# Optimization experiments

Hardware: AMD Instinct MI355X
Metric: run time of the kernel (lower is better)

Reference implementation:

```python
import jax, jax.numpy as jnp
import numpy as np

B, N, ENC = 64, 49, 1024
DEC, EMB, V = 512, 512, 10000
NT = 4            # num templates -> policy head dim = 1 + NT = 5
MS, MW = 8, 20    # max_sentences, max_words


def setup_inputs() -> dict:
    key = jax.random.key(0)
    ks = jax.random.split(key, 26)
    p = lambda k, shp: jax.random.normal(k, shp, dtype=jnp.float32) * 0.05
    return {
        'spatial_features': jax.random.normal(ks[0], (B, N, ENC), dtype=jnp.float32),
        'target_words': jax.random.randint(ks[1], (B, MS, MW), 0, V, dtype=jnp.int32),
        'emb_W': p(ks[2], (V, EMB)),
        's_W_ih': p(ks[3], (3 * DEC, ENC)),
        's_W_hh': p(ks[4], (3 * DEC, DEC)),
        's_b_ih': p(ks[5], (3 * DEC,)),
        's_b_hh': p(ks[6], (3 * DEC,)),
        'policy_W': p(ks[7], (1 + NT, DEC)),
        'policy_b': p(ks[8], (1 + NT,)),
        'stop_W': p(ks[9], (1, DEC)),
        'stop_b': p(ks[10], (1,)),
        'att_enc_W': p(ks[11], (EMB, ENC)),
        'att_enc_b': p(ks[12], (EMB,)),
        'att_dec_W': p(ks[13], (EMB, DEC)),
        'att_dec_b': p(ks[14], (EMB,)),
        'att_full_W': p(ks[15], (1, EMB)),
        'att_full_b': p(ks[16], (1,)),
        'w_W_ih': p(ks[17], (3 * DEC, EMB + ENC)),
        'w_W_hh': p(ks[18], (3 * DEC, DEC)),
        'w_b_ih': p(ks[19], (3 * DEC,)),
        'w_b_hh': p(ks[20], (3 * DEC,)),
        'fc_W': p(ks[21], (V, DEC)),
        'fc_b': p(ks[22], (V,)),
        'init_W': p(ks[23], (DEC, ENC)),
        'init_b': p(ks[24], (DEC,)),
    }


def _gru_cell(x, h, W_ih, W_hh, b_ih, b_hh):
    # torch.nn.GRUCell semantics
    gi = x @ W_ih.T + b_ih          # [B, 3D]
    gh = h @ W_hh.T + b_hh          # [B, 3D]
    i_r, i_z, i_n = jnp.split(gi, 3, axis=1)
    h_r, h_z, h_n = jnp.split(gh, 3, axis=1)
    r = jax.nn.sigmoid(i_r + h_r)
    z = jax.nn.sigmoid(i_z + h_z)
    n = jnp.tanh(i_n + r * h_n)
    return (1.0 - z) * n + z * h


def reference(spatial_features, target_words, emb_W,
              s_W_ih, s_W_hh, s_b_ih, s_b_hh,
              policy_W, policy_b, stop_W, stop_b,
              att_enc_W, att_enc_b, att_dec_W, att_dec_b, att_full_W, att_full_b,
              w_W_ih, w_W_hh, w_b_ih, w_b_hh,
              fc_W, fc_b, init_W, init_b):
    b = spatial_features.shape[0]
    global_features = spatial_features.mean(axis=1)                 # [B, ENC]
    h_s = jnp.tanh(global_features @ init_W.T + init_b)             # [B, DEC]
    # encoder attention projection is constant across all steps
    att1 = spatial_features @ att_enc_W.T + att_enc_b               # [B, N, EMB]

    def word_step(h_w, emb_t):
        att2 = h_w @ att_dec_W.T + att_dec_b                        # [B, EMB]
        e = jax.nn.relu(att1 + att2[:, None, :]) @ att_full_W[0] + att_full_b[0]  # [B, N]
        alpha = jax.nn.softmax(e, axis=1)
        ctx = jnp.einsum('bn,bnc->bc', alpha, spatial_features)     # [B, ENC]
        x = jnp.concatenate([emb_t, ctx], axis=1)                   # [B, EMB+ENC]
        h_new = _gru_cell(x, h_w, w_W_ih, w_W_hh, w_b_ih, w_b_hh)
        logits = h_new @ fc_W.T + fc_b                              # [B, V]
        return h_new, logits

    bos = jnp.full((b, 1), 1, dtype=target_words.dtype)
    policy_l, stop_l, word_l = [], [], []
    for i in range(MS):
        h_s = _gru_cell(global_features, h_s, s_W_ih, s_W_hh, s_b_ih, s_b_hh)
        policy_l.append(h_s @ policy_W.T + policy_b)
        stop_l.append(h_s @ stop_W.T + stop_b)
        # teacher forcing: input word at t is target[t-1], t=0 uses BOS(=1)
        prev = jnp.concatenate([bos, target_words[:, i, :-1]], axis=1)   # [B, MW]
        embs = jnp.swapaxes(emb_W[prev], 0, 1)                           # [MW, B, EMB]
        _, sent_logits = jax.lax.scan(word_step, h_s, embs)              # [MW, B, V]
        word_l.append(jnp.swapaxes(sent_logits, 0, 1))                   # [B, MW, V]

    return (jnp.stack(policy_l, axis=1),   # [B, MS, 1+NT]
            jnp.stack(stop_l, axis=1),     # [B, MS, 1]
            jnp.stack(word_l, axis=1))     # [B, MS, MW, V]
```

## Files before the change

### kernel.cpp

```cpp
#include <hip/hip_runtime.h>
#include <cmath>

constexpr int B = 64, N_SP = 49, ENC = 1024, DEC = 512, EMB = 512, V = 10000;
constexpr int MS = 8, MW = 20;
constexpr int BW = B * MS;
constexpr int XDIM = EMB + ENC;

__global__ void mean_kernel(const float* __restrict__ sp, float* __restrict__ g) {
    int b = blockIdx.x;
    for (int c = threadIdx.x; c < ENC; c += blockDim.x) {
        float s = 0.f;
        for (int n = 0; n < N_SP; ++n) s += sp[(size_t)(b * N_SP + n) * ENC + c];
        g[b * ENC + c] = s * (1.0f / 49.0f);
    }
}

template <int BM, int BN, int BK, int TM, int TN, int ACT, int SCATTER>
__launch_bounds__(256)
__global__ void gemm_tn(const float* __restrict__ A, int lda,
                        const float* __restrict__ W, int ldw,
                        const float* __restrict__ bias,
                        float* __restrict__ C, int ldc,
                        int M, int N, int K) {
    __shared__ float As[BK][BM + 4];
    __shared__ float Ws[BK][BN + 4];
    const int tid = threadIdx.x;
    const int tx = tid % (BN / TN);
    const int ty = tid / (BN / TN);
    const int m0 = blockIdx.y * BM, n0 = blockIdx.x * BN;

    float acc[TM][TN];
#pragma unroll
    for (int i = 0; i < TM; ++i)
#pragma unroll
        for (int j = 0; j < TN; ++j) acc[i][j] = 0.f;

    constexpr int Q = BK / 4;
    const int arow = tid / Q, akq = (tid % Q) * 4;
    const int wrow = tid / Q, wkq = (tid % Q) * 4;

    for (int k0 = 0; k0 < K; k0 += BK) {
        float4 av = make_float4(0.f, 0.f, 0.f, 0.f);
        float4 wv = make_float4(0.f, 0.f, 0.f, 0.f);
        int gr = m0 + arow;
        if (gr < M) av = *reinterpret_cast<const float4*>(&A[(size_t)gr * lda + k0 + akq]);
        int gn = n0 + wrow;
        if (gn < N) wv = *reinterpret_cast<const float4*>(&W[(size_t)gn * ldw + k0 + wkq]);
        __syncthreads();
        As[akq + 0][arow] = av.x; As[akq + 1][arow] = av.y;
        As[akq + 2][arow] = av.z; As[akq + 3][arow] = av.w;
        Ws[wkq + 0][wrow] = wv.x; Ws[wkq + 1][wrow] = wv.y;
        Ws[wkq + 2][wrow] = wv.z; Ws[wkq + 3][wrow] = wv.w;
        __syncthreads();
#pragma unroll
        for (int kk = 0; kk < BK; ++kk) {
            float a[TM], w[TN];
#pragma unroll
            for (int i = 0; i < TM; ++i) a[i] = As[kk][ty * TM + i];
#pragma unroll
            for (int j = 0; j < TN; ++j) w[j] = Ws[kk][tx * TN + j];
#pragma unroll
            for (int i = 0; i < TM; ++i)
#pragma unroll
                for (int j = 0; j < TN; ++j) acc[i][j] += a[i] * w[j];
        }
        __syncthreads();
    }

#pragma unroll
    for (int i = 0; i < TM; ++i) {
        int r = m0 + ty * TM + i;
        if (r >= M) continue;
#pragma unroll
        for (int j = 0; j < TN; ++j) {
            int n = n0 + tx * TN + j;
            if (n >= N) continue;
            float v = acc[i][j] + bias[n];
            if (ACT == 1) v = tanhf(v);
            size_t off;
            if (SCATTER) {
                int bb = r & 63, tt = (r >> 6) % MW, ss = r / (64 * MW);
                off = (size_t)((bb * MS + ss) * MW + tt) * ldc + n;
            } else {
                off = (size_t)r * ldc + n;
            }
            C[off] = v;
        }
    }
}

__global__ void gru_combine(const float* __restrict__ gi, const float* __restrict__ gh,
                            const float* __restrict__ hprev, float* __restrict__ hout,
                            float* __restrict__ hout2, int M, int t, int word_mode) {
    int idx = blockIdx.x * blockDim.x + threadIdx.x;
    if (idx >= M * DEC) return;
    int r = idx / DEC, c = idx % DEC;
    size_t g0 = (size_t)r * 3 * DEC + c;
    float ir = gi[g0], iz = gi[g0 + DEC], in_ = gi[g0 + 2 * DEC];
    float hr = gh[g0], hz = gh[g0 + DEC], hn = gh[g0 + 2 * DEC];
    float rr = 1.f / (1.f + expf(-(ir + hr)));
    float zz = 1.f / (1.f + expf(-(iz + hz)));
    float nn = tanhf(in_ + rr * hn);
    float h = (1.f - zz) * nn + zz * hprev[(size_t)r * DEC + c];
    hout[(size_t)r * DEC + c] = h;
    if (hout2) {
        int r2 = word_mode ? (((r >> 6) * MW + t) << 6) + (r & 63) : r;
        hout2[(size_t)r2 * DEC + c] = h;
    }
}

__launch_bounds__(256)
__global__ void attn_kernel(const float* __restrict__ sp, const float* __restrict__ att1,
                            const float* __restrict__ att2, const float* __restrict__ wfull,
                            const float* __restrict__ bfull, const float* __restrict__ embW,
                            const int* __restrict__ tw, float* __restrict__ x, int t) {
    int r = blockIdx.x;
    int s = r >> 6, b = r & 63;
    __shared__ float a2[EMB];
    __shared__ float wf[EMB];
    __shared__ float alpha[64];
    int tid = threadIdx.x;
    for (int c = tid; c < EMB; c += 256) {
        a2[c] = att2[(size_t)r * EMB + c];
        wf[c] = wfull[c];
    }
    __syncthreads();
    int wave = tid >> 6, lane = tid & 63;
    for (int n = wave; n < N_SP; n += 4) {
        float acc = 0.f;
        const float* a1p = &att1[(size_t)(b * N_SP + n) * EMB];
        for (int c0 = 0; c0 < EMB; c0 += 64) {
            float v = a1p[c0 + lane] + a2[c0 + lane];
            v = fmaxf(v, 0.f);
            acc += v * wf[c0 + lane];
        }
        for (int m = 32; m; m >>= 1) acc += __shfl_xor(acc, m, 64);
        if (lane == 0) alpha[n] = acc + bfull[0];
    }
    __syncthreads();
    if (tid < 64) {
        float e = (tid < N_SP) ? alpha[tid] : -1e30f;
        float mx = e;
        for (int m = 32; m; m >>= 1) mx = fmaxf(mx, __shfl_xor(mx, m, 64));
        float p = (tid < N_SP) ? expf(e - mx) : 0.f;
        float sum = p;
        for (int m = 32; m; m >>= 1) sum += __shfl_xor(sum, m, 64);
        if (tid < N_SP) alpha[tid] = p / sum;
    }
    __syncthreads();
    for (int c = tid; c < ENC; c += 256) {
        float acc = 0.f;
        const float* spb = &sp[(size_t)b * N_SP * ENC + c];
#pragma unroll 7
        for (int n = 0; n < N_SP; ++n) acc += alpha[n] * spb[(size_t)n * ENC];
        x[(size_t)r * XDIM + EMB + c] = acc;
    }
    int word = (t == 0) ? 1 : tw[b * (MS * MW) + s * MW + (t - 1)];
    for (int c = tid; c < EMB; c += 256) x[(size_t)r * XDIM + c] = embW[(size_t)word * EMB + c];
}

__launch_bounds__(64)
__global__ void policy_kernel(const float* __restrict__ hs_all, const float* __restrict__ pW,
                              const float* __restrict__ pb, const float* __restrict__ sW,
                              const float* __restrict__ sb, float* __restrict__ out) {
    int r = blockIdx.x;
    int s = r >> 6, b = r & 63;
    int lane = threadIdx.x;
    float acc[6] = {0.f, 0.f, 0.f, 0.f, 0.f, 0.f};
    for (int c = lane; c < DEC; c += 64) {
        float h = hs_all[(size_t)r * DEC + c];
#pragma unroll
        for (int j = 0; j < 5; ++j) acc[j] += h * pW[j * DEC + c];
        acc[5] += h * sW[c];
    }
#pragma unroll
    for (int j = 0; j < 6; ++j)
        for (int m = 32; m; m >>= 1) acc[j] += __shfl_xor(acc[j], m, 64);
    if (lane == 0) {
#pragma unroll
        for (int j = 0; j < 5; ++j) out[(b * MS + s) * 5 + j] = acc[j] + pb[j];
        out[B * MS * 5 + b * MS + s] = acc[5] + sb[0];
    }
}

extern "C" void kernel_launch(void* const* d_in, const int* in_sizes, int n_in,
                              void* d_out, int out_size, void* d_ws, size_t ws_size,
                              hipStream_t stream) {
    const float* sp   = (const float*)d_in[0];
    const int*   tw   = (const int*)d_in[1];
    const float* embW = (const float*)d_in[2];
    const float* sWih = (const float*)d_in[3];
    const float* sWhh = (const float*)d_in[4];
    const float* sbih = (const float*)d_in[5];
    const float* sbhh = (const float*)d_in[6];
    const float* pW   = (const float*)d_in[7];
    const float* pb   = (const float*)d_in[8];
    const float* stW  = (const float*)d_in[9];
    const float* stb  = (const float*)d_in[10];
    const float* aeW  = (const float*)d_in[11];
    const float* aeb  = (const float*)d_in[12];
    const float* adW  = (const float*)d_in[13];
    const float* adb  = (const float*)d_in[14];
    const float* afW  = (const float*)d_in[15];
    const float* afb  = (const float*)d_in[16];
    const float* wWih = (const float*)d_in[17];
    const float* wWhh = (const float*)d_in[18];
    const float* wbih = (const float*)d_in[19];
    const float* wbhh = (const float*)d_in[20];
    const float* fcW  = (const float*)d_in[21];
    const float* fcb  = (const float*)d_in[22];
    const float* iW   = (const float*)d_in[23];
    const float* ib   = (const float*)d_in[24];
    float* out = (float*)d_out;

    float* w = (float*)d_ws;
    float* g      = w; w += B * ENC;
    float* att1   = w; w += (size_t)B * N_SP * EMB;
    float* h_s    = w; w += B * DEC;
    float* gi_s   = w; w += B * 3 * DEC;
    float* gh_s   = w; w += B * 3 * DEC;
    float* h_sall = w; w += MS * B * DEC;
    float* xbuf   = w; w += (size_t)BW * XDIM;
    float* att2   = w; w += (size_t)BW * EMB;
    float* gib    = w; w += (size_t)BW * 3 * DEC;
    float* ghb    = w; w += (size_t)BW * 3 * DEC;
    float* h_all  = w; w += (size_t)MS * MW * B * DEC;
    float* h_w    = w; w += (size_t)BW * DEC;

    mean_kernel<<<B, 256, 0, stream>>>(sp, g);
    gemm_tn<64, 64, 16, 4, 4, 0, 0><<<dim3(512 / 64, (B * N_SP) / 64), 256, 0, stream>>>(
        sp, ENC, aeW, ENC, aeb, att1, EMB, B * N_SP, EMB, ENC);
    gemm_tn<64, 64, 16, 4, 4, 1, 0><<<dim3(512 / 64, 1), 256, 0, stream>>>(
        g, ENC, iW, ENC, ib, h_s, DEC, B, DEC, ENC);
    gemm_tn<64, 64, 16, 4, 4, 0, 0><<<dim3(1536 / 64, 1), 256, 0, stream>>>(
        g, ENC, sWih, ENC, sbih, gi_s, 3 * DEC, B, 3 * DEC, ENC);

    for (int i = 0; i < MS; ++i) {
        gemm_tn<64, 64, 16, 4, 4, 0, 0><<<dim3(1536 / 64, 1), 256, 0, stream>>>(
            h_s, DEC, sWhh, DEC, sbhh, gh_s, 3 * DEC, B, 3 * DEC, DEC);
        gru_combine<<<(B * DEC + 255) / 256, 256, 0, stream>>>(
            gi_s, gh_s, h_s, h_s, h_sall + (size_t)i * B * DEC, B, 0, 0);
    }
    policy_kernel<<<BW, 64, 0, stream>>>(h_sall, pW, pb, stW, stb, out);
    hipMemcpyAsync(h_w, h_sall, (size_t)BW * DEC * sizeof(float),
                   hipMemcpyDeviceToDevice, stream);

    for (int t = 0; t < MW; ++t) {
        gemm_tn<64, 64, 16, 4, 4, 0, 0><<<dim3(512 / 64, 512 / 64), 256, 0, stream>>>(
            h_w, DEC, adW, DEC, adb, att2, EMB, BW, EMB, DEC);
        attn_kernel<<<BW, 256, 0, stream>>>(sp, att1, att2, afW, afb, embW, tw, xbuf, t);
        gemm_tn<64, 64, 16, 4, 4, 0, 0><<<dim3(1536 / 64, 512 / 64), 256, 0, stream>>>(
            xbuf, XDIM, wWih, XDIM, wbih, gib, 3 * DEC, BW, 3 * DEC, XDIM);
        gemm_tn<64, 64, 16, 4, 4, 0, 0><<<dim3(1536 / 64, 512 / 64), 256, 0, stream>>>(
            h_w, DEC, wWhh, DEC, wbhh, ghb, 3 * DEC, BW, 3 * DEC, DEC);
        gru_combine<<<(BW * DEC + 255) / 256, 256, 0, stream>>>(
            gib, ghb, h_w, h_w, h_all, BW, t, 1);
    }

    gemm_tn<128, 128, 8, 8, 8, 0, 1><<<dim3((V + 127) / 128, (MS * MW * B) / 128), 256, 0, stream>>>(
        h_all, DEC, fcW, DEC, fcb, out + B * MS * 5 + B * MS, V, MS * MW * B, V, DEC);
}
```

Measured before the change: 5.964 ms.

## Persistent cooperative RNN kernel and bf16 MFMA output projection

Replaces the per-step launches of the sentence and word GRU loops with a single cooperative persistent kernel. It uses grid-wide syncs between phases, fuses the att2 and W_hh GEMMs into one phase, and batches attention across sentences per batch element. The large vocabulary projection moves from an fp32 SIMT GEMM to a bf16 MFMA kernel, with the fc weights converted to bf16 on every call and hidden states stored as bf16. This is meant to remove launch overhead and the cost of the dominant fp32 GEMM, at the price of reduced precision in the logits and a dependence on cooperative launch support, with a fallback path kept.

```diff
diff --git a/kernel.cpp b/kernel.cpp
--- a/kernel.cpp
+++ b/kernel.cpp
@@ -1,10 +1,24 @@
 #include <hip/hip_runtime.h>
+#include <hip/hip_cooperative_groups.h>
 #include <cmath>
+
+namespace cg = cooperative_groups;
 
 constexpr int B = 64, N_SP = 49, ENC = 1024, DEC = 512, EMB = 512, V = 10000;
 constexpr int MS = 8, MW = 20;
 constexpr int BW = B * MS;
 constexpr int XDIM = EMB + ENC;
+constexpr int GRID = 256;
+constexpr int NPAD = 10112;
+
+typedef __attribute__((ext_vector_type(8))) short short8v;
+typedef __attribute__((ext_vector_type(4))) float f32x4;
+
+__device__ __forceinline__ unsigned short f2bf(float f) {
+    union { float f; unsigned u; } x{f};
+    unsigned r = x.u + 0x7FFF + ((x.u >> 16) & 1);
+    return (unsigned short)(r >> 16);
+}
 
 __global__ void mean_kernel(const float* __restrict__ sp, float* __restrict__ g) {
     int b = blockIdx.x;
@@ -15,7 +29,7 @@
     }
 }
 
-template <int BM, int BN, int BK, int TM, int TN, int ACT, int SCATTER>
+template <int BM, int BN, int BK, int TM, int TN, int ACT>
 __launch_bounds__(256)
 __global__ void gemm_tn(const float* __restrict__ A, int lda,
                         const float* __restrict__ W, int ldw,
@@ -28,29 +42,25 @@
     const int tx = tid % (BN / TN);
     const int ty = tid / (BN / TN);
     const int m0 = blockIdx.y * BM, n0 = blockIdx.x * BN;
-
     float acc[TM][TN];
 #pragma unroll
     for (int i = 0; i < TM; ++i)
 #pragma unroll
         for (int j = 0; j < TN; ++j) acc[i][j] = 0.f;
-
     constexpr int Q = BK / 4;
     const int arow = tid / Q, akq = (tid % Q) * 4;
-    const int wrow = tid / Q, wkq = (tid % Q) * 4;
-
     for (int k0 = 0; k0 < K; k0 += BK) {
         float4 av = make_float4(0.f, 0.f, 0.f, 0.f);
         float4 wv = make_float4(0.f, 0.f, 0.f, 0.f);
         int gr = m0 + arow;
         if (gr < M) av = *reinterpret_cast<const float4*>(&A[(size_t)gr * lda + k0 + akq]);
-        int gn = n0 + wrow;
-        if (gn < N) wv = *reinterpret_cast<const float4*>(&W[(size_t)gn * ldw + k0 + wkq]);
+        int gn = n0 + arow;
+        if (gn < N) wv = *reinterpret_cast<const float4*>(&W[(size_t)gn * ldw + k0 + akq]);
         __syncthreads();
         As[akq + 0][arow] = av.x; As[akq + 1][arow] = av.y;
         As[akq + 2][arow] = av.z; As[akq + 3][arow] = av.w;
-        Ws[wkq + 0][wrow] = wv.x; Ws[wkq + 1][wrow] = wv.y;
-        Ws[wkq + 2][wrow] = wv.z; Ws[wkq + 3][wrow] = wv.w;
+        Ws[akq + 0][arow] = wv.x; Ws[akq + 1][arow] = wv.y;
+        Ws[akq + 2][arow] = wv.z; Ws[akq + 3][arow] = wv.w;
         __syncthreads();
 #pragma unroll
         for (int kk = 0; kk < BK; ++kk) {
@@ -66,7 +76,6 @@
         }
         __syncthreads();
     }
-
 #pragma unroll
     for (int i = 0; i < TM; ++i) {
         int r = m0 + ty * TM + i;
@@ -77,21 +86,15 @@
             if (n >= N) continue;
             float v = acc[i][j] + bias[n];
             if (ACT == 1) v = tanhf(v);
-            size_t off;
-            if (SCATTER) {
-                int bb = r & 63, tt = (r >> 6) % MW, ss = r / (64 * MW);
-                off = (size_t)((bb * MS + ss) * MW + tt) * ldc + n;
-            } else {
-                off = (size_t)r * ldc + n;
-            }
-            C[off] = v;
+            C[(size_t)r * ldc + n] = v;
         }
     }
 }
 
 __global__ void gru_combine(const float* __restrict__ gi, const float* __restrict__ gh,
                             const float* __restrict__ hprev, float* __restrict__ hout,
-                            float* __restrict__ hout2, int M, int t, int word_mode) {
+                            float* __restrict__ hout2, unsigned short* __restrict__ hout_bf,
+                            int M, int t) {
     int idx = blockIdx.x * blockDim.x + threadIdx.x;
     if (idx >= M * DEC) return;
     int r = idx / DEC, c = idx % DEC;
@@ -103,9 +106,10 @@
     float nn = tanhf(in_ + rr * hn);
     float h = (1.f - zz) * nn + zz * hprev[(size_t)r * DEC + c];
     hout[(size_t)r * DEC + c] = h;
-    if (hout2) {
-        int r2 = word_mode ? (((r >> 6) * MW + t) << 6) + (r & 63) : r;
-        hout2[(size_t)r2 * DEC + c] = h;
+    if (hout2) hout2[(size_t)r * DEC + c] = h;
+    if (hout_bf) {
+        int r2 = ((r >> 6) * MW + t) * 64 + (r & 63);
+        hout_bf[(size_t)r2 * DEC + c] = f2bf(h);
     }
 }
 
@@ -120,10 +124,7 @@
     __shared__ float wf[EMB];
     __shared__ float alpha[64];
     int tid = threadIdx.x;
-    for (int c = tid; c < EMB; c += 256) {
-        a2[c] = att2[(size_t)r * EMB + c];
-        wf[c] = wfull[c];
-    }
+    for (int c = tid; c < EMB; c += 256) { a2[c] = att2[(size_t)r * EMB + c]; wf[c] = wfull[c]; }
     __syncthreads();
     int wave = tid >> 6, lane = tid & 63;
     for (int n = wave; n < N_SP; n += 4) {
@@ -180,6 +181,311 @@
 #pragma unroll
         for (int j = 0; j < 5; ++j) out[(b * MS + s) * 5 + j] = acc[j] + pb[j];
         out[B * MS * 5 + b * MS + s] = acc[5] + sb[0];
+    }
+}
+
+__global__ void conv_w(const float* __restrict__ W, unsigned short* __restrict__ Wb,
+                       int rows, int validrows) {
+    for (size_t i = (size_t)blockIdx.x * 256 + threadIdx.x; i < (size_t)rows * DEC;
+         i += (size_t)gridDim.x * 256) {
+        int row = (int)(i >> 9);
+        Wb[i] = (row < validrows) ? f2bf(W[i]) : (unsigned short)0;
+    }
+}
+
+__global__ __launch_bounds__(256)
+void fc_mfma(const unsigned short* __restrict__ Ab,
+             const unsigned short* __restrict__ Wb,
+             const float* __restrict__ bias,
+             float* __restrict__ out) {
+    constexpr int K = 512, BK = 64, RS = 72;
+    __shared__ unsigned short As[128 * RS];
+    __shared__ unsigned short Bs[128 * RS];
+    const int tid = threadIdx.x;
+    const int m0 = blockIdx.y * 128, n0 = blockIdx.x * 128;
+    const int lane = tid & 63, wv = tid >> 6;
+    const int wm = (wv >> 1) * 64, wn = (wv & 1) * 64;
+    f32x4 acc[4][4];
+#pragma unroll
+    for (int i = 0; i < 4; ++i)
+#pragma unroll
+        for (int j = 0; j < 4; ++j) acc[i][j] = 0;
+
+    const int l15 = lane & 15, l4 = lane >> 4;
+    for (int k0 = 0; k0 < K; k0 += BK) {
+        __syncthreads();
+#pragma unroll
+        for (int q = 0; q < 4; ++q) {
+            int unit = q * 256 + tid;
+            int row = unit >> 3, u = unit & 7;
+            int4 va = *reinterpret_cast<const int4*>(&Ab[(size_t)(m0 + row) * K + k0 + u * 8]);
+            *reinterpret_cast<int4*>(&As[row * RS + u * 8]) = va;
+            int4 vb = *reinterpret_cast<const int4*>(&Wb[(size_t)(n0 + row) * K + k0 + u * 8]);
+            *reinterpret_cast<int4*>(&Bs[row * RS + u * 8]) = vb;
+        }
+        __syncthreads();
+#pragma unroll
+        for (int kb = 0; kb < 2; ++kb) {
+            short8v af[4], bf[4];
+#pragma unroll
+            for (int i = 0; i < 4; ++i)
+                af[i] = *reinterpret_cast<const short8v*>(
+                    &As[(wm + i * 16 + l15) * RS + kb * 32 + l4 * 8]);
+#pragma unroll
+            for (int j = 0; j < 4; ++j)
+                bf[j] = *reinterpret_cast<const short8v*>(
+                    &Bs[(wn + j * 16 + l15) * RS + kb * 32 + l4 * 8]);
+#pragma unroll
+            for (int i = 0; i < 4; ++i)
+#pragma unroll
+                for (int j = 0; j < 4; ++j)
+                    acc[i][j] = __builtin_amdgcn_mfma_f32_16x16x32_bf16(af[i], bf[j], acc[i][j], 0, 0, 0);
+        }
+    }
+    const int crow = l4 * 4;
+#pragma unroll
+    for (int i = 0; i < 4; ++i) {
+        int rgb = m0 + wm + i * 16 + crow;
+#pragma unroll
+        for (int j = 0; j < 4; ++j) {
+            int n_g = n0 + wn + j * 16 + l15;
+            if (n_g >= V) continue;
+            float bv = bias[n_g];
+#pragma unroll
+            for (int r = 0; r < 4; ++r) {
+                int rg = rgb + r;
+                int bb = rg & 63, tt = (rg >> 6) % MW, ss = rg / (64 * MW);
+                out[(size_t)((bb * MS + ss) * MW + tt) * V + n_g] = acc[i][j][r] + bv;
+            }
+        }
+    }
+}
+
+struct RnnParams {
+    const float* sp;
+    const float* embW;
+    const int* tw;
+    const float* sWhh; const float* sbhh;
+    const float* adW;  const float* adb;
+    const float* afW;  const float* afb;
+    const float* wWih; const float* wbih;
+    const float* wWhh; const float* wbhh;
+    const float* att1;
+    float* h_s; float* gi_s; float* gh_s; float* h_sall;
+    float* att2; float* xbuf; float* gib; float* ghb;
+    float* h_w;
+    unsigned short* h_all_bf;
+};
+
+__device__ __forceinline__ void gemm_tile64(
+    const float* __restrict__ A, int lda, const float* __restrict__ W, int ldw,
+    const float* __restrict__ bias, float* __restrict__ C, int ldc,
+    int m0, int n0, int K, float* smem) {
+    float (*As)[68] = reinterpret_cast<float(*)[68]>(smem);
+    float (*Ws)[68] = reinterpret_cast<float(*)[68]>(smem + 16 * 68);
+    const int tid = threadIdx.x;
+    const int tx = tid & 15, ty = tid >> 4;
+    const int lrow = tid >> 2, lkq = (tid & 3) << 2;
+    float acc[4][4] = {};
+    const float* Ap = A + (size_t)(m0 + lrow) * lda + lkq;
+    const float* Wp = W + (size_t)(n0 + lrow) * ldw + lkq;
+    for (int k0 = 0; k0 < K; k0 += 16) {
+        float4 av = *reinterpret_cast<const float4*>(Ap + k0);
+        float4 wv = *reinterpret_cast<const float4*>(Wp + k0);
+        __syncthreads();
+        As[lkq + 0][lrow] = av.x; As[lkq + 1][lrow] = av.y;
+        As[lkq + 2][lrow] = av.z; As[lkq + 3][lrow] = av.w;
+        Ws[lkq + 0][lrow] = wv.x; Ws[lkq + 1][lrow] = wv.y;
+        Ws[lkq + 2][lrow] = wv.z; Ws[lkq + 3][lrow] = wv.w;
+        __syncthreads();
+#pragma unroll
+        for (int kk = 0; kk < 16; ++kk) {
+            float a[4], w[4];
+#pragma unroll
+            for (int i = 0; i < 4; ++i) a[i] = As[kk][ty * 4 + i];
+#pragma unroll
+            for (int j = 0; j < 4; ++j) w[j] = Ws[kk][tx * 4 + j];
+#pragma unroll
+            for (int i = 0; i < 4; ++i)
+#pragma unroll
+                for (int j = 0; j < 4; ++j) acc[i][j] += a[i] * w[j];
+        }
+    }
+    __syncthreads();
+#pragma unroll
+    for (int i = 0; i < 4; ++i) {
+        float* Cp = C + (size_t)(m0 + ty * 4 + i) * ldc + n0 + tx * 4;
+#pragma unroll
+        for (int j = 0; j < 4; ++j) Cp[j] = acc[i][j] + bias[n0 + tx * 4 + j];
+    }
+}
+
+__device__ __forceinline__ void gemm_tile48(
+    const float* __restrict__ A, int lda, const float* __restrict__ W, int ldw,
+    const float* __restrict__ bias, float* __restrict__ C, int ldc,
+    int m0, int n0, int K, float* smem) {
+    float (*As)[68] = reinterpret_cast<float(*)[68]>(smem);
+    float (*Ws)[52] = reinterpret_cast<float(*)[52]>(smem + 16 * 68);
+    const int tid = threadIdx.x;
+    const int tx = tid & 15, ty = tid >> 4;
+    const int lrow = tid >> 2, lkq = (tid & 3) << 2;
+    const int wrow = tid >> 2;
+    float acc[4][3] = {};
+    const float* Ap = A + (size_t)(m0 + lrow) * lda + lkq;
+    const float* Wp = W + (size_t)(n0 + wrow) * ldw + lkq;
+    for (int k0 = 0; k0 < K; k0 += 16) {
+        float4 av = *reinterpret_cast<const float4*>(Ap + k0);
+        float4 wv = make_float4(0.f, 0.f, 0.f, 0.f);
+        if (tid < 192) wv = *reinterpret_cast<const float4*>(Wp + k0);
+        __syncthreads();
+        As[lkq + 0][lrow] = av.x; As[lkq + 1][lrow] = av.y;
+        As[lkq + 2][lrow] = av.z; As[lkq + 3][lrow] = av.w;
+        if (tid < 192) {
+            Ws[lkq + 0][wrow] = wv.x; Ws[lkq + 1][wrow] = wv.y;
+            Ws[lkq + 2][wrow] = wv.z; Ws[lkq + 3][wrow] = wv.w;
+        }
+        __syncthreads();
+#pragma unroll
+        for (int kk = 0; kk < 16; ++kk) {
+            float a[4], w[3];
+#pragma unroll
+            for (int i = 0; i < 4; ++i) a[i] = As[kk][ty * 4 + i];
+#pragma unroll
+            for (int j = 0; j < 3; ++j) w[j] = Ws[kk][tx * 3 + j];
+#pragma unroll
+            for (int i = 0; i < 4; ++i)
+#pragma unroll
+                for (int j = 0; j < 3; ++j) acc[i][j] += a[i] * w[j];
+        }
+    }
+    __syncthreads();
+#pragma unroll
+    for (int i = 0; i < 4; ++i) {
+        float* Cp = C + (size_t)(m0 + ty * 4 + i) * ldc + n0 + tx * 3;
+#pragma unroll
+        for (int j = 0; j < 3; ++j) Cp[j] = acc[i][j] + bias[n0 + tx * 3 + j];
+    }
+}
+
+__device__ __forceinline__ void attn_b(const RnnParams& p, int b, int t, float* smem) {
+    float* att2s = smem;
+    float* wf = smem + 4096;
+    float* ee = smem + 4608;
+    const int tid = threadIdx.x;
+    for (int i = tid; i < 8 * 512; i += 256) {
+        int s = i >> 9, c = i & 511;
+        att2s[i] = p.att2[(size_t)(s * 64 + b) * EMB + c];
+    }
+    for (int c = tid; c < 512; c += 256) wf[c] = p.afW[c];
+    __syncthreads();
+    const int wave = tid >> 6, lane = tid & 63;
+    for (int n = wave; n < N_SP; n += 4) {
+        const float* a1 = &p.att1[(size_t)(b * N_SP + n) * EMB];
+        float accs[8] = {};
+        for (int c0 = 0; c0 < 512; c0 += 64) {
+            float a1v = a1[c0 + lane];
+            float wfv = wf[c0 + lane];
+#pragma unroll
+            for (int s = 0; s < 8; ++s) {
+                float v = a1v + att2s[s * 512 + c0 + lane];
+                v = fmaxf(v, 0.f);
+                accs[s] += v * wfv;
+            }
+        }
+#pragma unroll
+        for (int s = 0; s < 8; ++s) {
+            float a = accs[s];
+            for (int m = 32; m; m >>= 1) a += __shfl_xor(a, m, 64);
+            if (lane == 0) ee[s * 64 + n] = a + p.afb[0];
+        }
+    }
+    __syncthreads();
+    for (int s = wave; s < 8; s += 4) {
+        float e = (lane < N_SP) ? ee[s * 64 + lane] : -1e30f;
+        float mx = e;
+        for (int m = 32; m; m >>= 1) mx = fmaxf(mx, __shfl_xor(mx, m, 64));
+        float pr = (lane < N_SP) ? expf(e - mx) : 0.f;
+        float sm = pr;
+        for (int m = 32; m; m >>= 1) sm += __shfl_xor(sm, m, 64);
+        if (lane < N_SP) ee[s * 64 + lane] = pr / sm;
+    }
+    __syncthreads();
+    for (int c = tid; c < ENC; c += 256) {
+        float acc0[8] = {};
+        const float* spb = &p.sp[(size_t)b * N_SP * ENC + c];
+        for (int n = 0; n < N_SP; ++n) {
+            float v = spb[(size_t)n * ENC];
+#pragma unroll
+            for (int s = 0; s < 8; ++s) acc0[s] += ee[s * 64 + n] * v;
+        }
+#pragma unroll
+        for (int s = 0; s < 8; ++s)
+            p.xbuf[(size_t)(s * 64 + b) * XDIM + EMB + c] = acc0[s];
+    }
+    for (int i = tid; i < 8 * 512; i += 256) {
+        int s = i >> 9, c = i & 511;
+        int word = (t == 0) ? 1 : p.tw[b * (MS * MW) + s * MW + (t - 1)];
+        p.xbuf[(size_t)(s * 64 + b) * XDIM + c] = p.embW[(size_t)word * EMB + c];
+    }
+    __syncthreads();
+}
+
+__global__ __launch_bounds__(256)
+void rnn_persistent(RnnParams p) {
+    cg::grid_group grid = cg::this_grid();
+    __shared__ float smem[5120];
+    const int wg = blockIdx.x;
+    const int tid = threadIdx.x;
+
+    for (int i = 0; i < MS; ++i) {
+        if (wg < 24)
+            gemm_tile64(p.h_s, DEC, p.sWhh, DEC, p.sbhh, p.gh_s, 3 * DEC, 0, wg * 64, DEC, smem);
+        grid.sync();
+        for (int idx = wg * 256 + tid; idx < B * DEC; idx += GRID * 256) {
+            int c = idx & 511, r = idx >> 9;
+            size_t g0 = (size_t)r * 3 * DEC + c;
+            float ir = p.gi_s[g0], iz = p.gi_s[g0 + DEC], in_ = p.gi_s[g0 + 2 * DEC];
+            float hr = p.gh_s[g0], hz = p.gh_s[g0 + DEC], hn = p.gh_s[g0 + 2 * DEC];
+            float rr = 1.f / (1.f + expf(-(ir + hr)));
+            float zz = 1.f / (1.f + expf(-(iz + hz)));
+            float nn = tanhf(in_ + rr * hn);
+            float h = (1.f - zz) * nn + zz * p.h_s[idx];
+            p.h_s[idx] = h;
+            p.h_sall[(size_t)i * B * DEC + idx] = h;
+            p.h_w[(size_t)i * B * DEC + idx] = h;
+        }
+        grid.sync();
+    }
+
+    for (int t = 0; t < MW; ++t) {
+        if (wg < 64)
+            gemm_tile64(p.h_w, DEC, p.adW, DEC, p.adb, p.att2, EMB,
+                        (wg >> 3) * 64, (wg & 7) * 64, DEC, smem);
+        else {
+            int j = wg - 64;
+            gemm_tile64(p.h_w, DEC, p.wWhh, DEC, p.wbhh, p.ghb, 3 * DEC,
+                        (j / 24) * 64, (j % 24) * 64, DEC, smem);
+        }
+        grid.sync();
+        if (wg < 64) attn_b(p, wg, t, smem);
+        grid.sync();
+        gemm_tile48(p.xbuf, XDIM, p.wWih, XDIM, p.wbih, p.gib, 3 * DEC,
+                    (wg >> 5) * 64, (wg & 31) * 48, XDIM, smem);
+        grid.sync();
+        for (int idx = wg * 256 + tid; idx < BW * DEC; idx += GRID * 256) {
+            int c = idx & 511, r = idx >> 9;
+            size_t g0 = (size_t)r * 3 * DEC + c;
+            float ir = p.gib[g0], iz = p.gib[g0 + DEC], in_ = p.gib[g0 + 2 * DEC];
+            float hr = p.ghb[g0], hz = p.ghb[g0 + DEC], hn = p.ghb[g0 + 2 * DEC];
+            float rr = 1.f / (1.f + expf(-(ir + hr)));
+            float zz = 1.f / (1.f + expf(-(iz + hz)));
+            float nn = tanhf(in_ + rr * hn);
+            float h = (1.f - zz) * nn + zz * p.h_w[idx];
+            p.h_w[idx] = h;
+            int r2 = ((r >> 6) * MW + t) * 64 + (r & 63);
+            p.h_all_bf[(size_t)r2 * DEC + c] = f2bf(h);
+        }
+        grid.sync();
     }
 }
 
@@ -224,39 +530,54 @@
     float* att2   = w; w += (size_t)BW * EMB;
     float* gib    = w; w += (size_t)BW * 3 * DEC;
     float* ghb    = w; w += (size_t)BW * 3 * DEC;
-    float* h_all  = w; w += (size_t)MS * MW * B * DEC;
     float* h_w    = w; w += (size_t)BW * DEC;
+    unsigned short* h_all_bf = (unsigned short*)w;
+    unsigned short* fcW_bf = h_all_bf + (size_t)MS * MW * B * DEC;
 
     mean_kernel<<<B, 256, 0, stream>>>(sp, g);
-    gemm_tn<64, 64, 16, 4, 4, 0, 0><<<dim3(512 / 64, (B * N_SP) / 64), 256, 0, stream>>>(
+    gemm_tn<64, 64, 16, 4, 4, 0><<<dim3(512 / 64, (B * N_SP) / 64), 256, 0, stream>>>(
         sp, ENC, aeW, ENC, aeb, att1, EMB, B * N_SP, EMB, ENC);
-    gemm_tn<64, 64, 16, 4, 4, 1, 0><<<dim3(512 / 64, 1), 256, 0, stream>>>(
+    gemm_tn<64, 64, 16, 4, 4, 1><<<dim3(512 / 64, 1), 256, 0, stream>>>(
         g, ENC, iW, ENC, ib, h_s, DEC, B, DEC, ENC);
-    gemm_tn<64, 64, 16, 4, 4, 0, 0><<<dim3(1536 / 64, 1), 256, 0, stream>>>(
+    gemm_tn<64, 64, 16, 4, 4, 0><<<dim3(1536 / 64, 1), 256, 0, stream>>>(
         g, ENC, sWih, ENC, sbih, gi_s, 3 * DEC, B, 3 * DEC, ENC);
-
-    for (int i = 0; i < MS; ++i) {
-        gemm_tn<64, 64, 16, 4, 4, 0, 0><<<dim3(1536 / 64, 1), 256, 0, stream>>>(
-            h_s, DEC, sWhh, DEC, sbhh, gh_s, 3 * DEC, B, 3 * DEC, DEC);
-        gru_combine<<<(B * DEC + 255) / 256, 256, 0, stream>>>(
-            gi_s, gh_s, h_s, h_s, h_sall + (size_t)i * B * DEC, B, 0, 0);
-    }
+    conv_w<<<1024, 256, 0, stream>>>(fcW, fcW_bf, NPAD, V);
+
+    RnnParams prm;
+    prm.sp = sp; prm.embW = embW; prm.tw = tw;
+    prm.sWhh = sWhh; prm.sbhh = sbhh;
+    prm.adW = adW; prm.adb = adb; prm.afW = afW; prm.afb = afb;
+    prm.wWih = wWih; prm.wbih = wbih; prm.wWhh = wWhh; prm.wbhh = wbhh;
+    prm.att1 = att1;
+    prm.h_s = h_s; prm.gi_s = gi_s; prm.gh_s = gh_s; prm.h_sall = h_sall;
+    prm.att2 = att2; prm.xbuf = xbuf; prm.gib = gib; prm.ghb = ghb;
+    prm.h_w = h_w; prm.h_all_bf = h_all_bf;
+    void* kargs[] = { (void*)&prm };
+    hipError_t cerr = hipLaunchCooperativeKernel(
+        reinterpret_cast<const void*>(&rnn_persistent), dim3(GRID), dim3(256), kargs, 0, stream);
+    if (cerr != hipSuccess) {
+        for (int i = 0; i < MS; ++i) {
+            gemm_tn<64, 64, 16, 4, 4, 0><<<dim3(1536 / 64, 1), 256, 0, stream>>>(
+                h_s, DEC, sWhh, DEC, sbhh, gh_s, 3 * DEC, B, 3 * DEC, DEC);
+            gru_combine<<<(B * DEC + 255) / 256, 256, 0, stream>>>(
+                gi_s, gh_s, h_s, h_s, h_sall + (size_t)i * B * DEC, nullptr, B, 0);
+        }
+        hipMemcpyAsync(h_w, h_sall, (size_t)BW * DEC * sizeof(float),
+                       hipMemcpyDeviceToDevice, stream);
+        for (int t = 0; t < MW; ++t) {
+            gemm_tn<64, 64, 16, 4, 4, 0><<<dim3(512 / 64, 512 / 64), 256, 0, stream>>>(
+                h_w, DEC, adW, DEC, adb, att2, EMB, BW, EMB, DEC);
+            attn_kernel<<<BW, 256, 0, stream>>>(sp, att1, att2, afW, afb, embW, tw, xbuf, t);
+            gemm_tn<64, 64, 16, 4, 4, 0><<<dim3(1536 / 64, 512 / 64), 256, 0, stream>>>(
+                xbuf, XDIM, wWih, XDIM, wbih, gib, 3 * DEC, BW, 3 * DEC, XDIM);
+            gemm_tn<64, 64, 16, 4, 4, 0><<<dim3(1536 / 64, 512 / 64), 256, 0, stream>>>(
+                h_w, DEC, wWhh, DEC, wbhh, ghb, 3 * DEC, BW, 3 * DEC, DEC);
+            gru_combine<<<(BW * DEC + 255) / 256, 256, 0, stream>>>(
+                gib, ghb, h_w, h_w, nullptr, h_all_bf, BW, t);
+        }
+    }
+
     policy_kernel<<<BW, 64, 0, stream>>>(h_sall, pW, pb, stW, stb, out);
-    hipMemcpyAsync(h_w, h_sall, (size_t)BW * DEC * sizeof(float),
-                   hipMemcpyDeviceToDevice, stream);
-
-    for (int t = 0; t < MW; ++t) {
-        gemm_tn<64, 64, 16, 4, 4, 0, 0><<<dim3(512 / 64, 512 / 64), 256, 0, stream>>>(
-            h_w, DEC, adW, DEC, adb, att2, EMB, BW, EMB, DEC);
-        attn_kernel<<<BW, 256, 0, stream>>>(sp, att1, att2, afW, afb, embW, tw, xbuf, t);
-        gemm_tn<64, 64, 16, 4, 4, 0, 0><<<dim3(1536 / 64, 512 / 64), 256, 0, stream>>>(
-            xbuf, XDIM, wWih, XDIM, wbih, gib, 3 * DEC, BW, 3 * DEC, XDIM);
-        gemm_tn<64, 64, 16, 4, 4, 0, 0><<<dim3(1536 / 64, 512 / 64), 256, 0, stream>>>(
-            h_w, DEC, wWhh, DEC, wbhh, ghb, 3 * DEC, BW, 3 * DEC, DEC);
-        gru_combine<<<(BW * DEC + 255) / 256, 256, 0, stream>>>(
-            gib, ghb, h_w, h_w, h_all, BW, t, 1);
-    }
-
-    gemm_tn<128, 128, 8, 8, 8, 0, 1><<<dim3((V + 127) / 128, (MS * MW * B) / 128), 256, 0, stream>>>(
-        h_all, DEC, fcW, DEC, fcb, out + B * MS * 5 + B * MS, V, MS * MW * B, V, DEC);
-}
+    fc_mfma<<<dim3(NPAD / 128, (MS * MW * B) / 128), 256, 0, stream>>>(
+        h_all_bf, fcW_bf, fcb, out + B * MS * 5 + B * MS);
+}
```

Result: slower. 7.979 ms (+33.8%).
